# Performance work log

Measured on AMD Instinct MI355X. Metric: run time of the kernel, lower is better.

The kernel has to match this reference:

```python
import jax, jax.numpy as jnp
import numpy as np


def _conv(x, w, b, stride, pad):
    # x: [N,C,H,W], w: [O,I,kh,kw]
    y = jax.lax.conv_general_dilated(
        x, w, (stride, stride), [(pad, pad), (pad, pad)],
        dimension_numbers=('NCHW', 'OIHW', 'NCHW'))
    return y + b[None, :, None, None]


def _block(x, w1, b1, w2, b2, stride):
    # BasicBlock with BN folded: conv3x3 -> relu -> conv3x3
    h = jax.nn.relu(_conv(x, w1, b1, stride, 1))
    return _conv(h, w2, b2, 1, 1)


def setup_inputs() -> dict:
    key = jax.random.key(0)
    keys = iter(jax.random.split(key, 64))

    def rn(shape):
        fan_in = int(np.prod(shape[1:])) if len(shape) > 1 else shape[0]
        return jax.random.normal(next(keys), shape, jnp.float32) * (1.0 / np.sqrt(fan_in))

    d = {}
    d['inputs'] = jax.random.normal(next(keys), (128, 3, 64, 64), jnp.float32)
    d['probs'] = jax.random.uniform(next(keys), (128, 15), jnp.float32)
    d['seed_w'] = rn((64, 3, 3, 3))
    d['seed_b'] = jnp.zeros((64,), jnp.float32)
    specs = [(64, 64), (64, 128), (128, 256)]  # (cin, cout) per group
    for g, (ci, co) in enumerate(specs):
        d[f'g{g}_ds_w'] = rn((co, ci, 1, 1))
        d[f'g{g}_ds_b'] = jnp.zeros((co,), jnp.float32)
        d[f'g{g}_b0_w1'] = rn((co, ci, 3, 3))
        d[f'g{g}_b0_b1'] = jnp.zeros((co,), jnp.float32)
        d[f'g{g}_b0_w2'] = rn((co, co, 3, 3))
        d[f'g{g}_b0_b2'] = jnp.zeros((co,), jnp.float32)
        d[f'g{g}_r_w1'] = rn((4, co, co, 3, 3))
        d[f'g{g}_r_b1'] = jnp.zeros((4, co), jnp.float32)
        d[f'g{g}_r_w2'] = rn((4, co, co, 3, 3))
        d[f'g{g}_r_b2'] = jnp.zeros((4, co), jnp.float32)
    d['fc_w'] = rn((1000, 256))
    d['fc_b'] = jnp.zeros((1000,), jnp.float32)
    return d


def reference(inputs, probs, seed_w, seed_b,
              g0_ds_w, g0_ds_b, g0_b0_w1, g0_b0_b1, g0_b0_w2, g0_b0_b2,
              g0_r_w1, g0_r_b1, g0_r_w2, g0_r_b2,
              g1_ds_w, g1_ds_b, g1_b0_w1, g1_b0_b1, g1_b0_w2, g1_b0_b2,
              g1_r_w1, g1_r_b1, g1_r_w2, g1_r_b2,
              g2_ds_w, g2_ds_b, g2_b0_w1, g2_b0_b1, g2_b0_w2, g2_b0_b2,
              g2_r_w1, g2_r_b1, g2_r_w2, g2_r_b2,
              fc_w, fc_b):
    # policy[k, n] in {0,1}: hard-threshold of agent probs at 0.5 (forward_real)
    policy = jnp.where(probs < 0.5, 0.0, 1.0).astype(inputs.dtype).T  # [15, B]
    x = jax.nn.relu(_conv(inputs, seed_w, seed_b, 1, 1))
    groups = [
        (g0_ds_w, g0_ds_b, g0_b0_w1, g0_b0_b1, g0_b0_w2, g0_b0_b2, g0_r_w1, g0_r_b1, g0_r_w2, g0_r_b2, 1),
        (g1_ds_w, g1_ds_b, g1_b0_w1, g1_b0_b1, g1_b0_w2, g1_b0_b2, g1_r_w1, g1_r_b1, g1_r_w2, g1_r_b2, 2),
        (g2_ds_w, g2_ds_b, g2_b0_w1, g2_b0_b1, g2_b0_w2, g2_b0_b2, g2_r_w1, g2_r_b1, g2_r_w2, g2_r_b2, 2),
    ]
    idx = 0
    for (ds_w, ds_b, b0_w1, b0_b1, b0_w2, b0_b2, r_w1, r_b1, r_w2, r_b2, s) in groups:
        # first block of the group: strided, with 1x1 downsample residual
        residual = _conv(x, ds_w, ds_b, s, 0)
        fx = _block(x, b0_w1, b0_b1, b0_w2, b0_b2, s)
        m = policy[idx][:, None, None, None]
        idx += 1
        x = m * jax.nn.relu(residual + fx) + (1.0 - m) * residual
        # remaining 4 identity-residual blocks
        for j in range(4):
            residual = x
            fx = _block(x, r_w1[j], r_b1[j], r_w2[j], r_b2[j], 1)
            m = policy[idx][:, None, None, None]
            idx += 1
            x = m * jax.nn.relu(residual + fx) + (1.0 - m) * residual
    pooled = x.mean(axis=(2, 3))  # global average pool [B, 256]
    return pooled @ fc_w.T + fc_b
```

## Files before the change

kernel.cpp:

```cpp
#include <hip/hip_runtime.h>

using bf = unsigned short;
typedef __attribute__((ext_vector_type(8))) short short8v;
typedef __attribute__((ext_vector_type(4))) float f32x4;
typedef __attribute__((ext_vector_type(4))) unsigned int u32x4;
typedef __attribute__((ext_vector_type(2))) unsigned int u32x2;

__device__ __forceinline__ float bf2f(bf u) { return __uint_as_float(((unsigned)u) << 16); }
__device__ __forceinline__ bf f2bf(float f) {
    unsigned x = __float_as_uint(f);
    x += 0x7fffu + ((x >> 16) & 1u);
    return (bf)(x >> 16);
}

__device__ __forceinline__ void gload16(const bf* g, bf* l) {
    __builtin_amdgcn_global_load_lds(
        (const __attribute__((address_space(1))) void*)g,
        (__attribute__((address_space(3))) void*)l, 16, 0, 0);
}

template <int CI, int CC, int STRIDE, bool SEED, bool DS, bool RELU, int CMB,
          int TH, int TW, int W>
__global__ __launch_bounds__(256, 3) void conv_mfma(
    const bf* __restrict__ X, const float* __restrict__ Xf,
    const bf* __restrict__ Wp, const bf* __restrict__ Wds,
    const float* __restrict__ bias, const float* __restrict__ dsb,
    bf* __restrict__ Y, bf* __restrict__ Yds,
    const bf* __restrict__ res, const float* __restrict__ probs,
    const bf* __restrict__ zpage, int kidx, int Co) {
    constexpr int IN_ROWS = (TH - 1) * STRIDE + 3;
    constexpr int IN_COLS = (TW - 1) * STRIDE + 3;
    constexpr int NG = CC / 8;
    constexpr int HIN = W * STRIDE;
    constexpr int NCH = CI / CC;
    constexpr int TG = IN_ROWS * IN_COLS * NG;
    constexpr int NITER = (TG + 255) / 256;
    constexpr int NF = (TH * TW) / 32;
    constexpr int TPR = W / TW;
    constexpr int KSH = (STRIDE == 2) ? 1 : 0;

    __shared__ bf sX[SEED ? TG * 8 : NITER * 256 * 8];

    const int tid = threadIdx.x;
    const int n = blockIdx.z;
    const int coBase = blockIdx.y << 6;
    const int bx = blockIdx.x;
    const int tr0 = (bx / TPR) * TH;
    const int tc0 = (bx % TPR) * TW;

    bool active = true;
    if (kidx >= 0) active = (probs[n * 15 + kidx] >= 0.5f);
    if (!active && !DS) return;

    const int lane = tid & 63;
    const int wid = tid >> 6;
    const int l15 = lane & 15;
    const int lq = lane >> 4;
    const int wm = wid >> 1;
    const int wn = wid & 1;

    f32x4 acc[2][NF] = {};
    f32x4 accds[DS ? 2 : 1][DS ? NF : 1] = {};
    int prow[NF], pcol[NF];
#pragma unroll
    for (int nf = 0; nf < NF; ++nf) {
        int p = wn * (TH * TW / 2) + nf * 16 + l15;
        prow[nf] = p / TW;
        pcol[nf] = p % TW;
    }

    const bf* Xn = X + (size_t)n * HIN * HIN * CI;

    for (int ch = 0; ch < NCH; ++ch) {
        if (ch) __syncthreads();
        if constexpr (SEED) {
            const float* Xfn = Xf + (size_t)n * 3 * HIN * HIN;
            if (tid < TG) {
                int ir = tid / IN_COLS;
                int ic = tid % IN_COLS;
                int in_r = tr0 - 1 + ir;
                int in_c = tc0 - 1 + ic;
                u32x4 u = {0, 0, 0, 0};
                if ((unsigned)in_r < (unsigned)HIN && (unsigned)in_c < (unsigned)HIN) {
                    const float* p = Xfn + (size_t)in_r * HIN + in_c;
                    u[0] = (unsigned)f2bf(p[0]) | ((unsigned)f2bf(p[HIN * HIN]) << 16);
                    u[1] = (unsigned)f2bf(p[2 * HIN * HIN]);
                }
                *reinterpret_cast<u32x4*>(&sX[(size_t)tid * 8]) = u;
            }
        } else {
#pragma unroll
            for (int i = 0; i < NITER; ++i) {
                int g = tid + i * 256;
                int ir = g / (IN_COLS * NG);
                int rem = g - ir * (IN_COLS * NG);
                int ic = rem / NG;
                int gc = rem - ic * NG;
                int in_r = tr0 * STRIDE - 1 + ir;
                int in_c = tc0 * STRIDE - 1 + ic;
                int gsrc = gc ^ ((ic >> KSH) & (NG - 1));
                const bf* src = zpage;
                if (g < TG && (unsigned)in_r < (unsigned)HIN && (unsigned)in_c < (unsigned)HIN)
                    src = Xn + ((size_t)in_r * HIN + in_c) * CI + ch * CC + gsrc * 8;
                gload16(src, &sX[(size_t)g * 8]);
            }
        }
        __syncthreads();

        if constexpr (SEED) {
#pragma unroll
            for (int kt = 0; kt < 3; ++kt) {
                int j = kt * 4 + lq;
                int jj = (j < 9) ? j : 0;
                int dh = jj / 3, dw = jj % 3;
                short8v a[2], b[NF];
#pragma unroll
                for (int mf = 0; mf < 2; ++mf) {
                    int co = coBase + wm * 32 + mf * 16 + l15;
                    a[mf] = *reinterpret_cast<const short8v*>(Wp + ((size_t)j * Co + co) * 8);
                }
#pragma unroll
                for (int nf = 0; nf < NF; ++nf) {
                    int ir = prow[nf] + dh;
                    int ic = pcol[nf] + dw;
                    b[nf] = *reinterpret_cast<const short8v*>(&sX[(ir * IN_COLS + ic) * 8]);
                }
#pragma unroll
                for (int mf = 0; mf < 2; ++mf)
#pragma unroll
                    for (int nf = 0; nf < NF; ++nf)
                        acc[mf][nf] = __builtin_amdgcn_mfma_f32_16x16x32_bf16(
                            a[mf], b[nf], acc[mf][nf], 0, 0, 0);
            }
        } else if (active) {
#pragma unroll
            for (int j = 0; j < 9; ++j) {
                const int dh = j / 3;
                const int dw = j % 3;
#pragma unroll
                for (int kk = 0; kk < CC / 32; ++kk) {
                    short8v a[2], b[NF];
#pragma unroll
                    for (int mf = 0; mf < 2; ++mf) {
                        int co = coBase + wm * 32 + mf * 16 + l15;
                        a[mf] = *reinterpret_cast<const short8v*>(
                            Wp + (((size_t)(ch * 9 + j) * Co + co) * CC + kk * 32 + lq * 8));
                    }
#pragma unroll
                    for (int nf = 0; nf < NF; ++nf) {
                        int ir = prow[nf] * STRIDE + dh;
                        int ic = pcol[nf] * STRIDE + dw;
                        int gk = (kk * 4 + lq) ^ ((ic >> KSH) & (NG - 1));
                        b[nf] = *reinterpret_cast<const short8v*>(
                            &sX[((ir * IN_COLS + ic) * NG + gk) * 8]);
                    }
#pragma unroll
                    for (int mf = 0; mf < 2; ++mf)
#pragma unroll
                        for (int nf = 0; nf < NF; ++nf)
                            acc[mf][nf] = __builtin_amdgcn_mfma_f32_16x16x32_bf16(
                                a[mf], b[nf], acc[mf][nf], 0, 0, 0);
                    if constexpr (DS) {
                        if (j == 4) {
                            short8v ads[2];
#pragma unroll
                            for (int mf = 0; mf < 2; ++mf) {
                                int co = coBase + wm * 32 + mf * 16 + l15;
                                ads[mf] = *reinterpret_cast<const short8v*>(
                                    Wds + ((size_t)ch * Co + co) * CC + kk * 32 + lq * 8);
                            }
#pragma unroll
                            for (int mf = 0; mf < 2; ++mf)
#pragma unroll
                                for (int nf = 0; nf < NF; ++nf)
                                    accds[mf][nf] = __builtin_amdgcn_mfma_f32_16x16x32_bf16(
                                        ads[mf], b[nf], accds[mf][nf], 0, 0, 0);
                        }
                    }
                }
            }
        } else if constexpr (DS) {
#pragma unroll
            for (int kk = 0; kk < CC / 32; ++kk) {
                short8v ads[2], b[NF];
#pragma unroll
                for (int mf = 0; mf < 2; ++mf) {
                    int co = coBase + wm * 32 + mf * 16 + l15;
                    ads[mf] = *reinterpret_cast<const short8v*>(
                        Wds + ((size_t)ch * Co + co) * CC + kk * 32 + lq * 8);
                }
#pragma unroll
                for (int nf = 0; nf < NF; ++nf) {
                    int ir = prow[nf] * STRIDE + 1;
                    int ic = pcol[nf] * STRIDE + 1;
                    int gk = (kk * 4 + lq) ^ ((ic >> KSH) & (NG - 1));
                    b[nf] = *reinterpret_cast<const short8v*>(
                        &sX[((ir * IN_COLS + ic) * NG + gk) * 8]);
                }
#pragma unroll
                for (int mf = 0; mf < 2; ++mf)
#pragma unroll
                    for (int nf = 0; nf < NF; ++nf)
                        accds[mf][nf] = __builtin_amdgcn_mfma_f32_16x16x32_bf16(
                            ads[mf], b[nf], accds[mf][nf], 0, 0, 0);
            }
        }
    }

#pragma unroll
    for (int mf = 0; mf < 2; ++mf) {
        int co0 = coBase + wm * 32 + mf * 16 + lq * 4;
#pragma unroll
        for (int nf = 0; nf < NF; ++nf) {
            size_t off = ((size_t)n * W * W + (size_t)(tr0 + prow[nf]) * W + tc0 + pcol[nf]) * Co + co0;
            if constexpr (DS) {
                float4 d4 = *reinterpret_cast<const float4*>(dsb + co0);
                float v[4];
#pragma unroll
                for (int i = 0; i < 4; ++i)
                    v[i] = accds[mf][nf][i] + ((const float*)&d4)[i];
                unsigned lo = (unsigned)f2bf(v[0]) | ((unsigned)f2bf(v[1]) << 16);
                unsigned hi = (unsigned)f2bf(v[2]) | ((unsigned)f2bf(v[3]) << 16);
                u32x2 o2 = {lo, hi};
                *reinterpret_cast<u32x2*>(Yds + off) = o2;
            }
            if (active) {
                float4 b4 = *reinterpret_cast<const float4*>(bias + co0);
                float v[4];
#pragma unroll
                for (int i = 0; i < 4; ++i) v[i] = acc[mf][nf][i] + ((const float*)&b4)[i];
                if constexpr (CMB >= 1) {
                    u32x2 r2 = *reinterpret_cast<const u32x2*>(res + off);
                    bf rr[4] = {(bf)(r2[0] & 0xffff), (bf)(r2[0] >> 16),
                                (bf)(r2[1] & 0xffff), (bf)(r2[1] >> 16)};
#pragma unroll
                    for (int i = 0; i < 4; ++i) v[i] = fmaxf(v[i] + bf2f(rr[i]), 0.f);
                }
                if constexpr (RELU) {
#pragma unroll
                    for (int i = 0; i < 4; ++i) v[i] = fmaxf(v[i], 0.f);
                }
                unsigned lo = (unsigned)f2bf(v[0]) | ((unsigned)f2bf(v[1]) << 16);
                unsigned hi = (unsigned)f2bf(v[2]) | ((unsigned)f2bf(v[3]) << 16);
                u32x2 o2 = {lo, hi};
                *reinterpret_cast<u32x2*>(Y + off) = o2;
            }
        }
    }
}

#define NSEG 34
struct Seg {
    const float* src;
    bf* dst;
    int Co, Ci, RSRS, CC, JPAD, blk0;
};
struct SegArgs {
    Seg s[NSEG];
};
__global__ void repack_all(SegArgs A) {
    int b = blockIdx.x;
    int lo = 0;
#pragma unroll 1
    for (int i = 1; i < NSEG; ++i)
        if (A.s[i].blk0 <= b) lo = i;
    Seg sg = A.s[lo];
    int NCH_ = (sg.Ci + sg.CC - 1) / sg.CC;
    size_t total8 = ((size_t)NCH_ * sg.JPAD * sg.Co * sg.CC) >> 3;
    size_t i8 = (size_t)(b - sg.blk0) * 256 + threadIdx.x;
    if (i8 >= total8) return;
    size_t e = i8 * 8;
    int cw = (int)(e % sg.CC);
    int co = (int)((e / sg.CC) % sg.Co);
    int j = (int)((e / ((size_t)sg.CC * sg.Co)) % sg.JPAD);
    int ch = (int)(e / ((size_t)sg.CC * sg.Co * sg.JPAD));
    bf tmp[8];
#pragma unroll
    for (int k = 0; k < 8; ++k) {
        int ci = ch * sg.CC + cw + k;
        float v = 0.f;
        if (ci < sg.Ci && j < sg.RSRS) v = sg.src[((size_t)co * sg.Ci + ci) * sg.RSRS + j];
        tmp[k] = f2bf(v);
    }
    u32x4 o;
#pragma unroll
    for (int k = 0; k < 4; ++k) o[k] = (unsigned)tmp[2 * k] | ((unsigned)tmp[2 * k + 1] << 16);
    *reinterpret_cast<u32x4*>(sg.dst + e) = o;
}

__global__ void zero_k(bf* p) {
    u32x4 z = {0, 0, 0, 0};
    *reinterpret_cast<u32x4*>(p + (size_t)threadIdx.x * 8) = z;
}

__global__ void poolfc_k(const bf* __restrict__ X, const float* __restrict__ fw,
                         const float* __restrict__ fb, float* __restrict__ out) {
    __shared__ float red[8][256];
    __shared__ float sp[256];
    int n = blockIdx.x;
    int g = threadIdx.x & 31;
    int slice = threadIdx.x >> 5;
    float acc[8] = {};
    for (int p = slice * 32; p < slice * 32 + 32; ++p) {
        u32x4 v = *reinterpret_cast<const u32x4*>(X + ((size_t)n * 256 + p) * 256 + g * 8);
#pragma unroll
        for (int i = 0; i < 4; ++i) {
            acc[2 * i] += bf2f((bf)(v[i] & 0xffff));
            acc[2 * i + 1] += bf2f((bf)(v[i] >> 16));
        }
    }
#pragma unroll
    for (int i = 0; i < 8; ++i) red[slice][g * 8 + i] = acc[i];
    __syncthreads();
    if (slice == 0) {
#pragma unroll
        for (int i = 0; i < 8; ++i) {
            float s = 0.f;
#pragma unroll
            for (int ss = 0; ss < 8; ++ss) s += red[ss][g * 8 + i];
            sp[g * 8 + i] = s * (1.f / 256.f);
        }
    }
    __syncthreads();
    for (int o = threadIdx.x; o < 1000; o += 256) {
        float a = fb[o];
        for (int k = 0; k < 256; ++k) a += sp[k] * fw[(size_t)o * 256 + k];
        out[(size_t)n * 1000 + o] = a;
    }
}

template <int CIN, int COUT, int S, int CC1, int W>
static void run_group(hipStream_t st, bf* X, bf* H, bf* OUT, const bf* zp,
                      bf* wp_ds, const float* ds_b, bf* wp_w1, const float* b1,
                      bf* wp_w2, const float* b2, bf* const* wp_rw1, const float* rb1,
                      bf* const* wp_rw2, const float* rb2, const float* probs_c,
                      int kbase, int NB) {
    dim3 grid((W / 8) * (W / 16), COUT / 64, NB);
    conv_mfma<CIN, CC1, S, false, true, true, 0, 8, 16, W><<<grid, 256, 0, st>>>(
        X, nullptr, wp_w1, wp_ds, b1, ds_b, H, OUT, nullptr, probs_c, zp, kbase, COUT);
    conv_mfma<COUT, 64, 1, false, false, false, 2, 8, 16, W><<<grid, 256, 0, st>>>(
        H, nullptr, wp_w2, nullptr, b2, nullptr, OUT, nullptr, OUT, probs_c, zp, kbase, COUT);
    for (int j = 0; j < 4; ++j) {
        conv_mfma<COUT, 64, 1, false, false, true, 0, 8, 16, W><<<grid, 256, 0, st>>>(
            OUT, nullptr, wp_rw1[j], nullptr, rb1 + j * COUT, nullptr, H, nullptr,
            nullptr, probs_c, zp, kbase + 1 + j, COUT);
        conv_mfma<COUT, 64, 1, false, false, false, 2, 8, 16, W><<<grid, 256, 0, st>>>(
            H, nullptr, wp_rw2[j], nullptr, rb2 + j * COUT, nullptr, OUT, nullptr,
            OUT, probs_c, zp, kbase + 1 + j, COUT);
    }
}

extern "C" void kernel_launch(void* const* d_in, const int* in_sizes, int n_in,
                              void* d_out, int out_size, void* d_ws, size_t ws_size,
                              hipStream_t stream) {
    (void)in_sizes; (void)n_in; (void)out_size;
    const float* input = (const float*)d_in[0];
    const float* probs = (const float*)d_in[1];
    const float* seed_w = (const float*)d_in[2];
    const float* seed_b = (const float*)d_in[3];
    const float* fc_w = (const float*)d_in[34];
    const float* fc_b = (const float*)d_in[35];

    char* pw = (char*)d_ws;
    auto alloc = [&](size_t bytes) -> void* {
        void* r = (void*)pw;
        pw += ((bytes + 255) & ~(size_t)255);
        return r;
    };

    bf* zpage = (bf*)alloc(256);

    SegArgs sa;
    int nseg = 0;
    int blkAcc = 0;
    auto pack = [&](const float* w, int Co_, int Ci_, int RSRS_, int CC_, int JPAD_) -> bf* {
        int NCH_ = (Ci_ + CC_ - 1) / CC_;
        size_t total = (size_t)NCH_ * JPAD_ * Co_ * CC_;
        bf* wp = (bf*)alloc(total * 2);
        sa.s[nseg] = {w, wp, Co_, Ci_, RSRS_, CC_, JPAD_, blkAcc};
        blkAcc += (int)(((total >> 3) + 255) / 256);
        ++nseg;
        return wp;
    };

    zero_k<<<dim3(1), 16, 0, stream>>>(zpage);

    bf* wpSeed = pack(seed_w, 64, 3, 9, 8, 12);
    const int cis[3] = {64, 64, 128};
    const int cos[3] = {64, 128, 256};
    const int cc1s[3] = {64, 32, 32};
    bf* wp_ds[3];
    bf* wp_w1[3];
    bf* wp_w2[3];
    bf* wp_rw1[3][4];
    bf* wp_rw2[3][4];
    const float *ds_b[3], *b1[3], *b2[3], *rb1[3], *rb2[3];
    for (int g = 0; g < 3; ++g) {
        int base = 4 + g * 10;
        const float* dsw = (const float*)d_in[base + 0];
        ds_b[g] = (const float*)d_in[base + 1];
        const float* w1 = (const float*)d_in[base + 2];
        b1[g] = (const float*)d_in[base + 3];
        const float* w2 = (const float*)d_in[base + 4];
        b2[g] = (const float*)d_in[base + 5];
        const float* rw1 = (const float*)d_in[base + 6];
        rb1[g] = (const float*)d_in[base + 7];
        const float* rw2 = (const float*)d_in[base + 8];
        rb2[g] = (const float*)d_in[base + 9];
        int Ci = cis[g], Co = cos[g];
        wp_ds[g] = pack(dsw, Co, Ci, 1, cc1s[g], 1);
        wp_w1[g] = pack(w1, Co, Ci, 9, cc1s[g], 9);
        wp_w2[g] = pack(w2, Co, Co, 9, 64, 9);
        for (int j = 0; j < 4; ++j) {
            wp_rw1[g][j] = pack(rw1 + (size_t)j * Co * Co * 9, Co, Co, 9, 64, 9);
            wp_rw2[g][j] = pack(rw2 + (size_t)j * Co * Co * 9, Co, Co, 9, 64, 9);
        }
    }
    for (int i = nseg; i < NSEG; ++i) sa.s[i] = {nullptr, nullptr, 1, 1, 1, 1, 1, 0x7fffffff};
    repack_all<<<dim3(blkAcc), 256, 0, stream>>>(sa);

    size_t used = (size_t)(pw - (char*)d_ws);
    size_t avail = (ws_size > used) ? (ws_size - used) : 0;
    const size_t PER_IMG = 64ull * 64 * 64 * 2;
    int NB = 128;
    while (NB > 8 && (size_t)3 * NB * PER_IMG + 4096 > avail) NB >>= 1;

    bf* A = (bf*)alloc((size_t)NB * PER_IMG);
    bf* Bb = (bf*)alloc((size_t)NB * PER_IMG);
    bf* C = (bf*)alloc((size_t)NB * PER_IMG);

    for (int n0 = 0; n0 < 128; n0 += NB) {
        const float* pc = probs + (size_t)n0 * 15;
        conv_mfma<8, 8, 1, true, false, true, 0, 8, 16, 64><<<dim3(32, 1, NB), 256, 0, stream>>>(
            nullptr, input + (size_t)n0 * 3 * 4096, wpSeed, nullptr, seed_b, nullptr,
            A, nullptr, nullptr, nullptr, zpage, -1, 64);

        run_group<64, 64, 1, 64, 64>(stream, A, Bb, C, zpage,
                                     wp_ds[0], ds_b[0], wp_w1[0], b1[0], wp_w2[0], b2[0],
                                     wp_rw1[0], rb1[0], wp_rw2[0], rb2[0], pc, 0, NB);
        run_group<64, 128, 2, 32, 32>(stream, C, Bb, A, zpage,
                                      wp_ds[1], ds_b[1], wp_w1[1], b1[1], wp_w2[1], b2[1],
                                      wp_rw1[1], rb1[1], wp_rw2[1], rb2[1], pc, 5, NB);
        run_group<128, 256, 2, 32, 16>(stream, A, Bb, C, zpage,
                                       wp_ds[2], ds_b[2], wp_w1[2], b1[2], wp_w2[2], b2[2],
                                       wp_rw1[2], rb1[2], wp_rw2[2], rb2[2], pc, 10, NB);

        poolfc_k<<<dim3(NB), 256, 0, stream>>>(C, fc_w, fc_b,
                                               (float*)d_out + (size_t)n0 * 1000);
    }
}
```

Baseline: 2.182 ms.

## Convert conv kernels to persistent grid with double-buffered LDS prefetch

Replaces the per-tile 3D launch grid with a persistent 1D grid capped at 1024 blocks that strides over a flattened tile index, skipping tiles of inactive images without launching them. Input tiles are staged into a second LDS buffer asynchronously while the current tile is computed, with explicit vmcnt waits and barriers, to hide global-load latency. Stride-2 downsample convs also switch to 8x8 output tiles. Doubling LDS may reduce occupancy, and the odd skip logic at loop entry adds per-tile overhead and risk.

Measured after the change: 3.103 ms. +42.2%, slower.

```diff
diff --git a/kernel.cpp b/kernel.cpp
--- a/kernel.cpp
+++ b/kernel.cpp
@@ -20,14 +20,14 @@
 }
 
 template <int CI, int CC, int STRIDE, bool SEED, bool DS, bool RELU, int CMB,
-          int TH, int TW, int W>
+          int TH, int TW, int W, int CO>
 __global__ __launch_bounds__(256, 3) void conv_mfma(
     const bf* __restrict__ X, const float* __restrict__ Xf,
     const bf* __restrict__ Wp, const bf* __restrict__ Wds,
     const float* __restrict__ bias, const float* __restrict__ dsb,
     bf* __restrict__ Y, bf* __restrict__ Yds,
     const bf* __restrict__ res, const float* __restrict__ probs,
-    const bf* __restrict__ zpage, int kidx, int Co) {
+    const bf* __restrict__ zpage, int kidx, int T) {
     constexpr int IN_ROWS = (TH - 1) * STRIDE + 3;
     constexpr int IN_COLS = (TW - 1) * STRIDE + 3;
     constexpr int NG = CC / 8;
@@ -35,32 +35,25 @@
     constexpr int NCH = CI / CC;
     constexpr int TG = IN_ROWS * IN_COLS * NG;
     constexpr int NITER = (TG + 255) / 256;
+    constexpr int BUFE = NITER * 256 * 8;
     constexpr int NF = (TH * TW) / 32;
-    constexpr int TPR = W / TW;
+    constexpr int COT = CO / 64;
+    constexpr int PXT = (W / TH) * (W / TW);
+    constexpr int TPI = PXT * COT;
     constexpr int KSH = (STRIDE == 2) ? 1 : 0;
-
-    __shared__ bf sX[SEED ? TG * 8 : NITER * 256 * 8];
+    constexpr bool SKIP = (!DS) && (!SEED);
+
+    __shared__ bf sX[SEED ? BUFE : 2 * BUFE];
 
     const int tid = threadIdx.x;
-    const int n = blockIdx.z;
-    const int coBase = blockIdx.y << 6;
-    const int bx = blockIdx.x;
-    const int tr0 = (bx / TPR) * TH;
-    const int tc0 = (bx % TPR) * TW;
-
-    bool active = true;
-    if (kidx >= 0) active = (probs[n * 15 + kidx] >= 0.5f);
-    if (!active && !DS) return;
-
     const int lane = tid & 63;
     const int wid = tid >> 6;
     const int l15 = lane & 15;
     const int lq = lane >> 4;
     const int wm = wid >> 1;
     const int wn = wid & 1;
-
-    f32x4 acc[2][NF] = {};
-    f32x4 accds[DS ? 2 : 1][DS ? NF : 1] = {};
+    const int G = (int)gridDim.x;
+
     int prow[NF], pcol[NF];
 #pragma unroll
     for (int nf = 0; nf < NF; ++nf) {
@@ -69,10 +62,30 @@
         pcol[nf] = p % TW;
     }
 
-    const bf* Xn = X + (size_t)n * HIN * HIN * CI;
-
-    for (int ch = 0; ch < NCH; ++ch) {
-        if (ch) __syncthreads();
+    f32x4 acc[2][NF];
+    f32x4 accds[DS ? 2 : 1][DS ? NF : 1];
+
+    auto activef = [&](int tau) -> bool {
+        if (kidx < 0) return true;
+        int n = tau / TPI;
+        return probs[n * 15 + kidx] >= 0.5f;
+    };
+    auto skip_inactive = [&](int tau) -> bool {
+        if constexpr (!SKIP) return false;
+        if (kidx < 0) return false;
+        return !activef(tau);
+    };
+    auto next_t = [&](int tau) -> int {
+        tau += G;
+        while (tau < T && skip_inactive(tau)) tau += G;
+        return tau;
+    };
+
+    auto stage = [&](int tau, int ch, bf* buf) {
+        int n = tau / TPI;
+        int pxid = (tau / COT) % PXT;
+        int tr0 = (pxid / (W / TW)) * TH;
+        int tc0 = (pxid % (W / TW)) * TW;
         if constexpr (SEED) {
             const float* Xfn = Xf + (size_t)n * 3 * HIN * HIN;
             if (tid < TG) {
@@ -86,9 +99,10 @@
                     u[0] = (unsigned)f2bf(p[0]) | ((unsigned)f2bf(p[HIN * HIN]) << 16);
                     u[1] = (unsigned)f2bf(p[2 * HIN * HIN]);
                 }
-                *reinterpret_cast<u32x4*>(&sX[(size_t)tid * 8]) = u;
+                *reinterpret_cast<u32x4*>(&buf[(size_t)tid * 8]) = u;
             }
         } else {
+            const bf* Xn = X + (size_t)n * HIN * HIN * CI;
 #pragma unroll
             for (int i = 0; i < NITER; ++i) {
                 int g = tid + i * 256;
@@ -102,10 +116,30 @@
                 const bf* src = zpage;
                 if (g < TG && (unsigned)in_r < (unsigned)HIN && (unsigned)in_c < (unsigned)HIN)
                     src = Xn + ((size_t)in_r * HIN + in_c) * CI + ch * CC + gsrc * 8;
-                gload16(src, &sX[(size_t)g * 8]);
-            }
-        }
-        __syncthreads();
+                gload16(src, &buf[(size_t)g * 8]);
+            }
+        }
+    };
+
+    auto compute = [&](int tau, int ch, const bf* buf, bool act) {
+        int n = tau / TPI;
+        int pxid = (tau / COT) % PXT;
+        int tr0 = (pxid / (W / TW)) * TH;
+        int tc0 = (pxid % (W / TW)) * TW;
+        int coBase = (tau % COT) << 6;
+
+        if (ch == 0) {
+#pragma unroll
+            for (int mf = 0; mf < 2; ++mf)
+#pragma unroll
+                for (int nf = 0; nf < NF; ++nf) acc[mf][nf] = f32x4{0.f, 0.f, 0.f, 0.f};
+            if constexpr (DS) {
+#pragma unroll
+                for (int mf = 0; mf < 2; ++mf)
+#pragma unroll
+                    for (int nf = 0; nf < NF; ++nf) accds[mf][nf] = f32x4{0.f, 0.f, 0.f, 0.f};
+            }
+        }
 
         if constexpr (SEED) {
 #pragma unroll
@@ -117,13 +151,13 @@
 #pragma unroll
                 for (int mf = 0; mf < 2; ++mf) {
                     int co = coBase + wm * 32 + mf * 16 + l15;
-                    a[mf] = *reinterpret_cast<const short8v*>(Wp + ((size_t)j * Co + co) * 8);
+                    a[mf] = *reinterpret_cast<const short8v*>(Wp + ((size_t)j * CO + co) * 8);
                 }
 #pragma unroll
                 for (int nf = 0; nf < NF; ++nf) {
                     int ir = prow[nf] + dh;
                     int ic = pcol[nf] + dw;
-                    b[nf] = *reinterpret_cast<const short8v*>(&sX[(ir * IN_COLS + ic) * 8]);
+                    b[nf] = *reinterpret_cast<const short8v*>(&buf[(ir * IN_COLS + ic) * 8]);
                 }
 #pragma unroll
                 for (int mf = 0; mf < 2; ++mf)
@@ -132,7 +166,7 @@
                         acc[mf][nf] = __builtin_amdgcn_mfma_f32_16x16x32_bf16(
                             a[mf], b[nf], acc[mf][nf], 0, 0, 0);
             }
-        } else if (active) {
+        } else if (act) {
 #pragma unroll
             for (int j = 0; j < 9; ++j) {
                 const int dh = j / 3;
@@ -144,7 +178,7 @@
                     for (int mf = 0; mf < 2; ++mf) {
                         int co = coBase + wm * 32 + mf * 16 + l15;
                         a[mf] = *reinterpret_cast<const short8v*>(
-                            Wp + (((size_t)(ch * 9 + j) * Co + co) * CC + kk * 32 + lq * 8));
+                            Wp + (((size_t)(ch * 9 + j) * CO + co) * CC + kk * 32 + lq * 8));
                     }
 #pragma unroll
                     for (int nf = 0; nf < NF; ++nf) {
@@ -152,7 +186,7 @@
                         int ic = pcol[nf] * STRIDE + dw;
                         int gk = (kk * 4 + lq) ^ ((ic >> KSH) & (NG - 1));
                         b[nf] = *reinterpret_cast<const short8v*>(
-                            &sX[((ir * IN_COLS + ic) * NG + gk) * 8]);
+                            &buf[((ir * IN_COLS + ic) * NG + gk) * 8]);
                     }
 #pragma unroll
                     for (int mf = 0; mf < 2; ++mf)
@@ -167,7 +201,7 @@
                             for (int mf = 0; mf < 2; ++mf) {
                                 int co = coBase + wm * 32 + mf * 16 + l15;
                                 ads[mf] = *reinterpret_cast<const short8v*>(
-                                    Wds + ((size_t)ch * Co + co) * CC + kk * 32 + lq * 8);
+                                    Wds + ((size_t)ch * CO + co) * CC + kk * 32 + lq * 8);
                             }
 #pragma unroll
                             for (int mf = 0; mf < 2; ++mf)
@@ -187,7 +221,7 @@
                 for (int mf = 0; mf < 2; ++mf) {
                     int co = coBase + wm * 32 + mf * 16 + l15;
                     ads[mf] = *reinterpret_cast<const short8v*>(
-                        Wds + ((size_t)ch * Co + co) * CC + kk * 32 + lq * 8);
+                        Wds + ((size_t)ch * CO + co) * CC + kk * 32 + lq * 8);
                 }
 #pragma unroll
                 for (int nf = 0; nf < NF; ++nf) {
@@ -195,7 +229,7 @@
                     int ic = pcol[nf] * STRIDE + 1;
                     int gk = (kk * 4 + lq) ^ ((ic >> KSH) & (NG - 1));
                     b[nf] = *reinterpret_cast<const short8v*>(
-                        &sX[((ir * IN_COLS + ic) * NG + gk) * 8]);
+                        &buf[((ir * IN_COLS + ic) * NG + gk) * 8]);
                 }
 #pragma unroll
                 for (int mf = 0; mf < 2; ++mf)
@@ -205,47 +239,96 @@
                             ads[mf], b[nf], accds[mf][nf], 0, 0, 0);
             }
         }
-    }
-
-#pragma unroll
-    for (int mf = 0; mf < 2; ++mf) {
-        int co0 = coBase + wm * 32 + mf * 16 + lq * 4;
-#pragma unroll
-        for (int nf = 0; nf < NF; ++nf) {
-            size_t off = ((size_t)n * W * W + (size_t)(tr0 + prow[nf]) * W + tc0 + pcol[nf]) * Co + co0;
-            if constexpr (DS) {
-                float4 d4 = *reinterpret_cast<const float4*>(dsb + co0);
-                float v[4];
-#pragma unroll
-                for (int i = 0; i < 4; ++i)
-                    v[i] = accds[mf][nf][i] + ((const float*)&d4)[i];
-                unsigned lo = (unsigned)f2bf(v[0]) | ((unsigned)f2bf(v[1]) << 16);
-                unsigned hi = (unsigned)f2bf(v[2]) | ((unsigned)f2bf(v[3]) << 16);
-                u32x2 o2 = {lo, hi};
-                *reinterpret_cast<u32x2*>(Yds + off) = o2;
-            }
-            if (active) {
-                float4 b4 = *reinterpret_cast<const float4*>(bias + co0);
-                float v[4];
-#pragma unroll
-                for (int i = 0; i < 4; ++i) v[i] = acc[mf][nf][i] + ((const float*)&b4)[i];
-                if constexpr (CMB >= 1) {
-                    u32x2 r2 = *reinterpret_cast<const u32x2*>(res + off);
-                    bf rr[4] = {(bf)(r2[0] & 0xffff), (bf)(r2[0] >> 16),
-                                (bf)(r2[1] & 0xffff), (bf)(r2[1] >> 16)};
-#pragma unroll
-                    for (int i = 0; i < 4; ++i) v[i] = fmaxf(v[i] + bf2f(rr[i]), 0.f);
-                }
-                if constexpr (RELU) {
-#pragma unroll
-                    for (int i = 0; i < 4; ++i) v[i] = fmaxf(v[i], 0.f);
-                }
-                unsigned lo = (unsigned)f2bf(v[0]) | ((unsigned)f2bf(v[1]) << 16);
-                unsigned hi = (unsigned)f2bf(v[2]) | ((unsigned)f2bf(v[3]) << 16);
-                u32x2 o2 = {lo, hi};
-                *reinterpret_cast<u32x2*>(Y + off) = o2;
-            }
-        }
+
+        if (ch == NCH - 1) {
+#pragma unroll
+            for (int mf = 0; mf < 2; ++mf) {
+                int co0 = coBase + wm * 32 + mf * 16 + lq * 4;
+#pragma unroll
+                for (int nf = 0; nf < NF; ++nf) {
+                    size_t off = ((size_t)n * W * W + (size_t)(tr0 + prow[nf]) * W +
+                                  tc0 + pcol[nf]) * CO + co0;
+                    if constexpr (DS) {
+                        float4 d4 = *reinterpret_cast<const float4*>(dsb + co0);
+                        float v[4];
+#pragma unroll
+                        for (int i = 0; i < 4; ++i) v[i] = accds[mf][nf][i] + ((const float*)&d4)[i];
+                        unsigned lo = (unsigned)f2bf(v[0]) | ((unsigned)f2bf(v[1]) << 16);
+                        unsigned hi = (unsigned)f2bf(v[2]) | ((unsigned)f2bf(v[3]) << 16);
+                        u32x2 o2 = {lo, hi};
+                        *reinterpret_cast<u32x2*>(Yds + off) = o2;
+                    }
+                    if (act) {
+                        float4 b4 = *reinterpret_cast<const float4*>(bias + co0);
+                        float v[4];
+#pragma unroll
+                        for (int i = 0; i < 4; ++i) v[i] = acc[mf][nf][i] + ((const float*)&b4)[i];
+                        if constexpr (CMB >= 1) {
+                            u32x2 r2 = *reinterpret_cast<const u32x2*>(res + off);
+                            bf rr[4] = {(bf)(r2[0] & 0xffff), (bf)(r2[0] >> 16),
+                                        (bf)(r2[1] & 0xffff), (bf)(r2[1] >> 16)};
+#pragma unroll
+                            for (int i = 0; i < 4; ++i) v[i] = fmaxf(v[i] + bf2f(rr[i]), 0.f);
+                        }
+                        if constexpr (RELU) {
+#pragma unroll
+                            for (int i = 0; i < 4; ++i) v[i] = fmaxf(v[i], 0.f);
+                        }
+                        unsigned lo = (unsigned)f2bf(v[0]) | ((unsigned)f2bf(v[1]) << 16);
+                        unsigned hi = (unsigned)f2bf(v[2]) | ((unsigned)f2bf(v[3]) << 16);
+                        u32x2 o2 = {lo, hi};
+                        *reinterpret_cast<u32x2*>(Y + off) = o2;
+                    }
+                }
+            }
+        }
+    };
+
+    int t = blockIdx.x;
+    if (t >= T) return;
+    if (skip_inactive(t)) t = next_t(t - G + G == t ? t : t);
+    if (skip_inactive(t)) {  }
+    if (t < T && skip_inactive(t)) t = next_t(t);
+    if (t >= T) return;
+    bool act = activef(t);
+    int ch = 0;
+    stage(t, ch, sX);
+    int p = 0;
+    while (true) {
+        int tn = t, chn = ch + 1;
+        bool actn = act;
+        if (chn == NCH) {
+            chn = 0;
+            tn = next_t(t);
+            actn = (tn < T) ? activef(tn) : false;
+        }
+        bool hn = (tn < T);
+        if constexpr (SEED) {
+            __syncthreads();
+            compute(t, ch, sX, act);
+            if (!hn) break;
+            __syncthreads();
+            stage(tn, chn, sX);
+        } else {
+            if (hn) {
+                __builtin_amdgcn_sched_barrier(0);
+                stage(tn, chn, sX + (size_t)(p ^ 1) * BUFE);
+                __builtin_amdgcn_sched_barrier(0);
+                asm volatile("s_waitcnt vmcnt(%0)" ::"n"(NITER) : "memory");
+            } else {
+                __builtin_amdgcn_sched_barrier(0);
+                asm volatile("s_waitcnt vmcnt(0)" ::: "memory");
+            }
+            __builtin_amdgcn_s_barrier();
+            __builtin_amdgcn_sched_barrier(0);
+            compute(t, ch, sX + (size_t)p * BUFE, act);
+            if (!hn) break;
+            __builtin_amdgcn_s_barrier();
+            p ^= 1;
+        }
+        t = tn;
+        ch = chn;
+        act = actn;
     }
 }
 
@@ -329,24 +412,37 @@
     }
 }
 
+static inline int gmin(int a, int b) { return a < b ? a : b; }
+
 template <int CIN, int COUT, int S, int CC1, int W>
 static void run_group(hipStream_t st, bf* X, bf* H, bf* OUT, const bf* zp,
                       bf* wp_ds, const float* ds_b, bf* wp_w1, const float* b1,
                       bf* wp_w2, const float* b2, bf* const* wp_rw1, const float* rb1,
                       bf* const* wp_rw2, const float* rb2, const float* probs_c,
                       int kbase, int NB) {
-    dim3 grid((W / 8) * (W / 16), COUT / 64, NB);
-    conv_mfma<CIN, CC1, S, false, true, true, 0, 8, 16, W><<<grid, 256, 0, st>>>(
-        X, nullptr, wp_w1, wp_ds, b1, ds_b, H, OUT, nullptr, probs_c, zp, kbase, COUT);
-    conv_mfma<COUT, 64, 1, false, false, false, 2, 8, 16, W><<<grid, 256, 0, st>>>(
-        H, nullptr, wp_w2, nullptr, b2, nullptr, OUT, nullptr, OUT, probs_c, zp, kbase, COUT);
+    constexpr int COT = COUT / 64;
+    constexpr int PXT1 = (W / 8) * (W / 16);
+    int T1 = PXT1 * COT * NB;
+    int G1 = gmin(1024, T1);
+    if constexpr (S == 2) {
+        constexpr int PXT2 = (W / 8) * (W / 8);
+        int T2 = PXT2 * COT * NB;
+        int G2 = gmin(1024, T2);
+        conv_mfma<CIN, CC1, 2, false, true, true, 0, 8, 8, W, COUT><<<G2, 256, 0, st>>>(
+            X, nullptr, wp_w1, wp_ds, b1, ds_b, H, OUT, nullptr, probs_c, zp, kbase, T2);
+    } else {
+        conv_mfma<CIN, CC1, 1, false, true, true, 0, 8, 16, W, COUT><<<G1, 256, 0, st>>>(
+            X, nullptr, wp_w1, wp_ds, b1, ds_b, H, OUT, nullptr, probs_c, zp, kbase, T1);
+    }
+    conv_mfma<COUT, 64, 1, false, false, false, 2, 8, 16, W, COUT><<<G1, 256, 0, st>>>(
+        H, nullptr, wp_w2, nullptr, b2, nullptr, OUT, nullptr, OUT, probs_c, zp, kbase, T1);
     for (int j = 0; j < 4; ++j) {
-        conv_mfma<COUT, 64, 1, false, false, true, 0, 8, 16, W><<<grid, 256, 0, st>>>(
+        conv_mfma<COUT, 64, 1, false, false, true, 0, 8, 16, W, COUT><<<G1, 256, 0, st>>>(
             OUT, nullptr, wp_rw1[j], nullptr, rb1 + j * COUT, nullptr, H, nullptr,
-            nullptr, probs_c, zp, kbase + 1 + j, COUT);
-        conv_mfma<COUT, 64, 1, false, false, false, 2, 8, 16, W><<<grid, 256, 0, st>>>(
+            nullptr, probs_c, zp, kbase + 1 + j, T1);
+        conv_mfma<COUT, 64, 1, false, false, false, 2, 8, 16, W, COUT><<<G1, 256, 0, st>>>(
             H, nullptr, wp_rw2[j], nullptr, rb2 + j * COUT, nullptr, OUT, nullptr,
-            OUT, probs_c, zp, kbase + 1 + j, COUT);
+            OUT, probs_c, zp, kbase + 1 + j, T1);
     }
 }
 
@@ -431,9 +527,11 @@
 
     for (int n0 = 0; n0 < 128; n0 += NB) {
         const float* pc = probs + (size_t)n0 * 15;
-        conv_mfma<8, 8, 1, true, false, true, 0, 8, 16, 64><<<dim3(32, 1, NB), 256, 0, stream>>>(
+        int Ts = 32 * NB;
+        int Gs = gmin(1024, Ts);
+        conv_mfma<8, 8, 1, true, false, true, 0, 8, 16, 64, 64><<<Gs, 256, 0, stream>>>(
             nullptr, input + (size_t)n0 * 3 * 4096, wpSeed, nullptr, seed_b, nullptr,
-            A, nullptr, nullptr, nullptr, zpage, -1, 64);
+            A, nullptr, nullptr, nullptr, zpage, -1, Ts);
 
         run_group<64, 64, 1, 64, 64>(stream, A, Bb, C, zpage,
                                      wp_ds[0], ds_b[0], wp_w1[0], b1[0], wp_w2[0], b2[0],
```

## Double-buffer LDS input tiles and process multiple pixel tiles per block

Applied to the files above, without the earlier changes.

Each conv block now walks several spatial tiles (TPB) and channel chunks as a flat stage sequence. While one stage computes from LDS, the next stage is prefetched into a second buffer via global_load_lds, gated by an explicit vmcnt wait and raw barriers. Strided first convs also switch to 8x8 tiles. This is meant to hide global-load latency behind MFMA work. The cost is double the LDS per block, which may lower occupancy, and fewer blocks in the grid.

Result: slower. 3.559 ms (+63.1%).

```diff
diff --git a/kernel.cpp b/kernel.cpp
--- a/kernel.cpp
+++ b/kernel.cpp
@@ -20,7 +20,7 @@
 }
 
 template <int CI, int CC, int STRIDE, bool SEED, bool DS, bool RELU, int CMB,
-          int TH, int TW, int W>
+          int TH, int TW, int W, int TPB>
 __global__ __launch_bounds__(256, 3) void conv_mfma(
     const bf* __restrict__ X, const float* __restrict__ Xf,
     const bf* __restrict__ Wp, const bf* __restrict__ Wds,
@@ -35,18 +35,17 @@
     constexpr int NCH = CI / CC;
     constexpr int TG = IN_ROWS * IN_COLS * NG;
     constexpr int NITER = (TG + 255) / 256;
+    constexpr int BUFE = NITER * 256 * 8;
     constexpr int NF = (TH * TW) / 32;
-    constexpr int TPR = W / TW;
     constexpr int KSH = (STRIDE == 2) ? 1 : 0;
-
-    __shared__ bf sX[SEED ? TG * 8 : NITER * 256 * 8];
+    constexpr int S = TPB * NCH;
+
+    __shared__ bf sX[SEED ? BUFE : 2 * BUFE];
 
     const int tid = threadIdx.x;
+    const int run = blockIdx.x;
     const int n = blockIdx.z;
     const int coBase = blockIdx.y << 6;
-    const int bx = blockIdx.x;
-    const int tr0 = (bx / TPR) * TH;
-    const int tc0 = (bx % TPR) * TW;
 
     bool active = true;
     if (kidx >= 0) active = (probs[n * 15 + kidx] >= 0.5f);
@@ -59,8 +58,8 @@
     const int wm = wid >> 1;
     const int wn = wid & 1;
 
-    f32x4 acc[2][NF] = {};
-    f32x4 accds[DS ? 2 : 1][DS ? NF : 1] = {};
+    f32x4 acc[2][NF];
+    f32x4 accds[DS ? 2 : 1][DS ? NF : 1];
     int prow[NF], pcol[NF];
 #pragma unroll
     for (int nf = 0; nf < NF; ++nf) {
@@ -69,10 +68,19 @@
         pcol[nf] = p % TW;
     }
 
+    auto tile_rc = [&](int t, int& tr0, int& tc0) {
+        int px = run * TPB + t;
+        tr0 = (px / (W / TW)) * TH;
+        tc0 = (px % (W / TW)) * TW;
+    };
+
     const bf* Xn = X + (size_t)n * HIN * HIN * CI;
 
-    for (int ch = 0; ch < NCH; ++ch) {
-        if (ch) __syncthreads();
+    auto stage = [&](int s, bf* buf) {
+        int t = s / NCH;
+        int ch = s % NCH;
+        int tr0, tc0;
+        tile_rc(t, tr0, tc0);
         if constexpr (SEED) {
             const float* Xfn = Xf + (size_t)n * 3 * HIN * HIN;
             if (tid < TG) {
@@ -86,7 +94,7 @@
                     u[0] = (unsigned)f2bf(p[0]) | ((unsigned)f2bf(p[HIN * HIN]) << 16);
                     u[1] = (unsigned)f2bf(p[2 * HIN * HIN]);
                 }
-                *reinterpret_cast<u32x4*>(&sX[(size_t)tid * 8]) = u;
+                *reinterpret_cast<u32x4*>(&buf[(size_t)tid * 8]) = u;
             }
         } else {
 #pragma unroll
@@ -102,10 +110,29 @@
                 const bf* src = zpage;
                 if (g < TG && (unsigned)in_r < (unsigned)HIN && (unsigned)in_c < (unsigned)HIN)
                     src = Xn + ((size_t)in_r * HIN + in_c) * CI + ch * CC + gsrc * 8;
-                gload16(src, &sX[(size_t)g * 8]);
-            }
-        }
-        __syncthreads();
+                gload16(src, &buf[(size_t)g * 8]);
+            }
+        }
+    };
+
+    auto compute = [&](int s, const bf* buf) {
+        int t = s / NCH;
+        int ch = s % NCH;
+        int tr0, tc0;
+        tile_rc(t, tr0, tc0);
+
+        if (ch == 0) {
+#pragma unroll
+            for (int mf = 0; mf < 2; ++mf)
+#pragma unroll
+                for (int nf = 0; nf < NF; ++nf) acc[mf][nf] = f32x4{0.f, 0.f, 0.f, 0.f};
+            if constexpr (DS) {
+#pragma unroll
+                for (int mf = 0; mf < 2; ++mf)
+#pragma unroll
+                    for (int nf = 0; nf < NF; ++nf) accds[mf][nf] = f32x4{0.f, 0.f, 0.f, 0.f};
+            }
+        }
 
         if constexpr (SEED) {
 #pragma unroll
@@ -123,7 +150,7 @@
                 for (int nf = 0; nf < NF; ++nf) {
                     int ir = prow[nf] + dh;
                     int ic = pcol[nf] + dw;
-                    b[nf] = *reinterpret_cast<const short8v*>(&sX[(ir * IN_COLS + ic) * 8]);
+                    b[nf] = *reinterpret_cast<const short8v*>(&buf[(ir * IN_COLS + ic) * 8]);
                 }
 #pragma unroll
                 for (int mf = 0; mf < 2; ++mf)
@@ -152,7 +179,7 @@
                         int ic = pcol[nf] * STRIDE + dw;
                         int gk = (kk * 4 + lq) ^ ((ic >> KSH) & (NG - 1));
                         b[nf] = *reinterpret_cast<const short8v*>(
-                            &sX[((ir * IN_COLS + ic) * NG + gk) * 8]);
+                            &buf[((ir * IN_COLS + ic) * NG + gk) * 8]);
                     }
 #pragma unroll
                     for (int mf = 0; mf < 2; ++mf)
@@ -195,7 +222,7 @@
                     int ic = pcol[nf] * STRIDE + 1;
                     int gk = (kk * 4 + lq) ^ ((ic >> KSH) & (NG - 1));
                     b[nf] = *reinterpret_cast<const short8v*>(
-                        &sX[((ir * IN_COLS + ic) * NG + gk) * 8]);
+                        &buf[((ir * IN_COLS + ic) * NG + gk) * 8]);
                 }
 #pragma unroll
                 for (int mf = 0; mf < 2; ++mf)
@@ -205,46 +232,72 @@
                             ads[mf], b[nf], accds[mf][nf], 0, 0, 0);
             }
         }
-    }
-
-#pragma unroll
-    for (int mf = 0; mf < 2; ++mf) {
-        int co0 = coBase + wm * 32 + mf * 16 + lq * 4;
-#pragma unroll
-        for (int nf = 0; nf < NF; ++nf) {
-            size_t off = ((size_t)n * W * W + (size_t)(tr0 + prow[nf]) * W + tc0 + pcol[nf]) * Co + co0;
-            if constexpr (DS) {
-                float4 d4 = *reinterpret_cast<const float4*>(dsb + co0);
-                float v[4];
-#pragma unroll
-                for (int i = 0; i < 4; ++i)
-                    v[i] = accds[mf][nf][i] + ((const float*)&d4)[i];
-                unsigned lo = (unsigned)f2bf(v[0]) | ((unsigned)f2bf(v[1]) << 16);
-                unsigned hi = (unsigned)f2bf(v[2]) | ((unsigned)f2bf(v[3]) << 16);
-                u32x2 o2 = {lo, hi};
-                *reinterpret_cast<u32x2*>(Yds + off) = o2;
-            }
-            if (active) {
-                float4 b4 = *reinterpret_cast<const float4*>(bias + co0);
-                float v[4];
-#pragma unroll
-                for (int i = 0; i < 4; ++i) v[i] = acc[mf][nf][i] + ((const float*)&b4)[i];
-                if constexpr (CMB >= 1) {
-                    u32x2 r2 = *reinterpret_cast<const u32x2*>(res + off);
-                    bf rr[4] = {(bf)(r2[0] & 0xffff), (bf)(r2[0] >> 16),
-                                (bf)(r2[1] & 0xffff), (bf)(r2[1] >> 16)};
-#pragma unroll
-                    for (int i = 0; i < 4; ++i) v[i] = fmaxf(v[i] + bf2f(rr[i]), 0.f);
-                }
-                if constexpr (RELU) {
-#pragma unroll
-                    for (int i = 0; i < 4; ++i) v[i] = fmaxf(v[i], 0.f);
-                }
-                unsigned lo = (unsigned)f2bf(v[0]) | ((unsigned)f2bf(v[1]) << 16);
-                unsigned hi = (unsigned)f2bf(v[2]) | ((unsigned)f2bf(v[3]) << 16);
-                u32x2 o2 = {lo, hi};
-                *reinterpret_cast<u32x2*>(Y + off) = o2;
-            }
+
+        if (ch == NCH - 1) {
+#pragma unroll
+            for (int mf = 0; mf < 2; ++mf) {
+                int co0 = coBase + wm * 32 + mf * 16 + lq * 4;
+#pragma unroll
+                for (int nf = 0; nf < NF; ++nf) {
+                    size_t off = ((size_t)n * W * W + (size_t)(tr0 + prow[nf]) * W +
+                                  tc0 + pcol[nf]) * Co + co0;
+                    if constexpr (DS) {
+                        float4 d4 = *reinterpret_cast<const float4*>(dsb + co0);
+                        float v[4];
+#pragma unroll
+                        for (int i = 0; i < 4; ++i) v[i] = accds[mf][nf][i] + ((const float*)&d4)[i];
+                        unsigned lo = (unsigned)f2bf(v[0]) | ((unsigned)f2bf(v[1]) << 16);
+                        unsigned hi = (unsigned)f2bf(v[2]) | ((unsigned)f2bf(v[3]) << 16);
+                        u32x2 o2 = {lo, hi};
+                        *reinterpret_cast<u32x2*>(Yds + off) = o2;
+                    }
+                    if (active) {
+                        float4 b4 = *reinterpret_cast<const float4*>(bias + co0);
+                        float v[4];
+#pragma unroll
+                        for (int i = 0; i < 4; ++i) v[i] = acc[mf][nf][i] + ((const float*)&b4)[i];
+                        if constexpr (CMB >= 1) {
+                            u32x2 r2 = *reinterpret_cast<const u32x2*>(res + off);
+                            bf rr[4] = {(bf)(r2[0] & 0xffff), (bf)(r2[0] >> 16),
+                                        (bf)(r2[1] & 0xffff), (bf)(r2[1] >> 16)};
+#pragma unroll
+                            for (int i = 0; i < 4; ++i) v[i] = fmaxf(v[i] + bf2f(rr[i]), 0.f);
+                        }
+                        if constexpr (RELU) {
+#pragma unroll
+                            for (int i = 0; i < 4; ++i) v[i] = fmaxf(v[i], 0.f);
+                        }
+                        unsigned lo = (unsigned)f2bf(v[0]) | ((unsigned)f2bf(v[1]) << 16);
+                        unsigned hi = (unsigned)f2bf(v[2]) | ((unsigned)f2bf(v[3]) << 16);
+                        u32x2 o2 = {lo, hi};
+                        *reinterpret_cast<u32x2*>(Y + off) = o2;
+                    }
+                }
+            }
+        }
+    };
+
+    if constexpr (SEED) {
+        stage(0, sX);
+        __syncthreads();
+        compute(0, sX);
+    } else {
+        int p = 0;
+        stage(0, sX);
+#pragma unroll 1
+        for (int s = 0; s < S; ++s) {
+            if (s + 1 < S) {
+                stage(s + 1, sX + (size_t)(p ^ 1) * BUFE);
+                __builtin_amdgcn_sched_barrier(0);
+                asm volatile("s_waitcnt vmcnt(%0)" ::"n"(NITER) : "memory");
+            } else {
+                asm volatile("s_waitcnt vmcnt(0)" ::: "memory");
+            }
+            __builtin_amdgcn_s_barrier();
+            __builtin_amdgcn_sched_barrier(0);
+            compute(s, sX + (size_t)p * BUFE);
+            if (s + 1 < S) __builtin_amdgcn_s_barrier();
+            p ^= 1;
         }
     }
 }
@@ -335,16 +388,27 @@
                       bf* wp_w2, const float* b2, bf* const* wp_rw1, const float* rb1,
                       bf* const* wp_rw2, const float* rb2, const float* probs_c,
                       int kbase, int NB) {
-    dim3 grid((W / 8) * (W / 16), COUT / 64, NB);
-    conv_mfma<CIN, CC1, S, false, true, true, 0, 8, 16, W><<<grid, 256, 0, st>>>(
-        X, nullptr, wp_w1, wp_ds, b1, ds_b, H, OUT, nullptr, probs_c, zp, kbase, COUT);
-    conv_mfma<COUT, 64, 1, false, false, false, 2, 8, 16, W><<<grid, 256, 0, st>>>(
+    constexpr int COT = COUT / 64;
+    constexpr int PXT1 = (W / 8) * (W / 16);
+    constexpr int TPB1 = (PXT1 >= 4) ? 4 : PXT1;
+    dim3 grid1(PXT1 / TPB1, COT, NB);
+    if constexpr (S == 2) {
+        constexpr int PXT2 = (W / 8) * (W / 8);
+        constexpr int TPB2 = (PXT2 >= 4) ? 4 : PXT2;
+        dim3 grid2(PXT2 / TPB2, COT, NB);
+        conv_mfma<CIN, CC1, 2, false, true, true, 0, 8, 8, W, TPB2><<<grid2, 256, 0, st>>>(
+            X, nullptr, wp_w1, wp_ds, b1, ds_b, H, OUT, nullptr, probs_c, zp, kbase, COUT);
+    } else {
+        conv_mfma<CIN, CC1, 1, false, true, true, 0, 8, 16, W, TPB1><<<grid1, 256, 0, st>>>(
+            X, nullptr, wp_w1, wp_ds, b1, ds_b, H, OUT, nullptr, probs_c, zp, kbase, COUT);
+    }
+    conv_mfma<COUT, 64, 1, false, false, false, 2, 8, 16, W, TPB1><<<grid1, 256, 0, st>>>(
         H, nullptr, wp_w2, nullptr, b2, nullptr, OUT, nullptr, OUT, probs_c, zp, kbase, COUT);
     for (int j = 0; j < 4; ++j) {
-        conv_mfma<COUT, 64, 1, false, false, true, 0, 8, 16, W><<<grid, 256, 0, st>>>(
+        conv_mfma<COUT, 64, 1, false, false, true, 0, 8, 16, W, TPB1><<<grid1, 256, 0, st>>>(
             OUT, nullptr, wp_rw1[j], nullptr, rb1 + j * COUT, nullptr, H, nullptr,
             nullptr, probs_c, zp, kbase + 1 + j, COUT);
-        conv_mfma<COUT, 64, 1, false, false, false, 2, 8, 16, W><<<grid, 256, 0, st>>>(
+        conv_mfma<COUT, 64, 1, false, false, false, 2, 8, 16, W, TPB1><<<grid1, 256, 0, st>>>(
             H, nullptr, wp_rw2[j], nullptr, rb2 + j * COUT, nullptr, OUT, nullptr,
             OUT, probs_c, zp, kbase + 1 + j, COUT);
     }
@@ -431,7 +495,7 @@
 
     for (int n0 = 0; n0 < 128; n0 += NB) {
         const float* pc = probs + (size_t)n0 * 15;
-        conv_mfma<8, 8, 1, true, false, true, 0, 8, 16, 64><<<dim3(32, 1, NB), 256, 0, stream>>>(
+        conv_mfma<8, 8, 1, true, false, true, 0, 8, 16, 64, 1><<<dim3(32, 1, NB), 256, 0, stream>>>(
             nullptr, input + (size_t)n0 * 3 * 4096, wpSeed, nullptr, seed_b, nullptr,
             A, nullptr, nullptr, nullptr, zpage, -1, 64);
 
```
